# Kernel tuning notes

Hardware: AMD Instinct MI355X
Metric: run time of the kernel (lower is better)

The kernel has to match this reference:

```python
import jax, jax.numpy as jnp
import numpy as np

N, IN_F, OUT_F = 8192, 512, 128
NEG = -1e11
LRELU_SLOPE = 0.01  # torch nn.LeakyReLU default


def setup_inputs() -> dict:
    key = jax.random.key(0)
    k1, k2, k3, k4, k5 = jax.random.split(key, 5)
    h = jax.random.normal(k1, (N, IN_F), dtype=jnp.float32)
    adj = jax.random.randint(k2, (N, N), 0, 2, dtype=jnp.int32)
    # nn.Linear weights, [out, in] convention; kaiming-uniform-ish init
    w = jax.random.uniform(k3, (OUT_F, IN_F), dtype=jnp.float32,
                           minval=-1.0, maxval=1.0) / np.sqrt(IN_F)
    a1 = jax.random.uniform(k4, (1, OUT_F), dtype=jnp.float32,
                            minval=-1.0, maxval=1.0) / np.sqrt(OUT_F)
    a2 = jax.random.uniform(k5, (1, OUT_F), dtype=jnp.float32,
                            minval=-1.0, maxval=1.0) / np.sqrt(OUT_F)
    return {"h": h, "adj": adj, "w": w, "a1": a1, "a2": a2}


def reference(h, adj, w, a1, a2):
    wh = h @ w.T                                # [N, out]
    wh1 = wh @ a1.T                             # [N, 1]
    wh2 = wh @ a2.T                             # [N, 1]
    e = wh1 + wh2.T                             # [N, N] broadcast add
    e = jnp.where(e > 0, e, LRELU_SLOPE * e)    # leaky relu
    scores = jnp.where(adj > 0, e, jnp.float32(NEG))
    attention = jax.nn.softmax(scores, axis=-1)  # [N, N]
    h_new = attention @ wh                       # [N, out]
    return jax.nn.elu(h_new)
```

## Files before the change

kernel.cpp:

```cpp
#include <hip/hip_runtime.h>
#include <hip/hip_bf16.h>
#include <cstdint>
#include <cstddef>

#define NV    8192
#define KIN   512
#define MOUT  128
#define LOG2E 1.4426950408889634f

typedef __attribute__((ext_vector_type(4))) float f32x4;
typedef __attribute__((ext_vector_type(8))) short short8;

__device__ __forceinline__ float elu1(float x) { return x > 0.f ? x : expm1f(x); }

__device__ __forceinline__ unsigned int pkbf2(float a, float b) {
  union { __hip_bfloat162 h2; unsigned int u; } r;
  r.h2 = __float22bfloat162_rn(make_float2(a, b));
  return r.u;
}

__global__ __launch_bounds__(256) void k_wh(const float* __restrict__ h,
                                            const float* __restrict__ w,
                                            const float* __restrict__ a1,
                                            const float* __restrict__ a2,
                                            unsigned short* __restrict__ fragB,
                                            float* __restrict__ wh1,
                                            float* __restrict__ wh2) {
  __shared__ __align__(16) float hT[64][36];
  __shared__ __align__(16) float wT[64][128];
  const int t = threadIdx.x;
  const int row0 = blockIdx.x * 32;
  const int hr = t >> 3, hu = t & 7;
  const int wc = t >> 1, whalf = t & 1;
  const int cg = t & 31, rg = t >> 5;
  const int c0 = cg * 4, r0 = rg * 4;
  float acc[4][4] = {};

  for (int kt = 0; kt < 8; ++kt) {
    const int k0 = kt * 64;
    __syncthreads();
#pragma unroll
    for (int v = 0; v < 8; ++v)
      hT[hu + 8 * v][hr] = h[(size_t)(row0 + hr) * KIN + k0 + hu + 8 * v];
#pragma unroll
    for (int mv = 0; mv < 8; ++mv) {
      const float4 wv4 = *(const float4*)&w[(size_t)wc * KIN + k0 + whalf * 32 + mv * 4];
      wT[whalf * 32 + mv * 4 + 0][wc] = wv4.x;
      wT[whalf * 32 + mv * 4 + 1][wc] = wv4.y;
      wT[whalf * 32 + mv * 4 + 2][wc] = wv4.z;
      wT[whalf * 32 + mv * 4 + 3][wc] = wv4.w;
    }
    __syncthreads();
#pragma unroll 8
    for (int kk = 0; kk < 64; ++kk) {
      const float4 hv = *(const float4*)&hT[kk][r0];
      const float4 wv4 = *(const float4*)&wT[kk][c0];
      const float hvv[4] = {hv.x, hv.y, hv.z, hv.w};
      const float wvv[4] = {wv4.x, wv4.y, wv4.z, wv4.w};
#pragma unroll
      for (int i = 0; i < 4; ++i)
#pragma unroll
        for (int j = 0; j < 4; ++j)
          acc[i][j] = fmaf(hvv[i], wvv[j], acc[i][j]);
    }
  }

  {
    const size_t jt = (size_t)(row0 >> 6);
    const int ks = (row0 >> 5) & 1;
    const int lg = rg >> 1, ebase = (rg & 1) * 4;
    const int cgf = cg >> 2;
    const size_t fbase = (((jt * 8 + cgf) * 2 + ks) * 64 + lg * 16) * 8 + ebase;
#pragma unroll
    for (int j = 0; j < 4; ++j) {
      const int l15 = (cg & 3) * 4 + j;
      uint2 o;
      o.x = pkbf2(acc[0][j], acc[1][j]);
      o.y = pkbf2(acc[2][j], acc[3][j]);
      *(uint2*)&fragB[fbase + (size_t)l15 * 8] = o;
    }
  }

  const float4 a1v = *(const float4*)&a1[c0];
  const float4 a2v = *(const float4*)&a2[c0];
#pragma unroll
  for (int i = 0; i < 4; ++i) {
    float s1 = acc[i][0] * a1v.x + acc[i][1] * a1v.y + acc[i][2] * a1v.z + acc[i][3] * a1v.w;
    float s2 = acc[i][0] * a2v.x + acc[i][1] * a2v.y + acc[i][2] * a2v.z + acc[i][3] * a2v.w;
#pragma unroll
    for (int off = 16; off > 0; off >>= 1) {
      s1 += __shfl_down(s1, off, 32);
      s2 += __shfl_down(s2, off, 32);
    }
    if (cg == 0) {
      wh1[row0 + r0 + i] = s1 * LOG2E;
      wh2[row0 + r0 + i] = s2 * LOG2E;
    }
  }
}

__global__ __launch_bounds__(256) void k_attn_p(const unsigned short* __restrict__ fragB,
                                                const int* __restrict__ adj,
                                                const float* __restrict__ wh1l,
                                                const float* __restrict__ wh2l,
                                                float* __restrict__ out_p,
                                                float* __restrict__ psum_p,
                                                int ntiles) {
  __shared__ char smask[64 * 136];
  const int t = threadIdx.x;
  const int i0 = blockIdx.x * 64;
  const int jbase = blockIdx.y * ntiles * 64;
  const int lane = t & 63, wv = t >> 6;
  const int ih = wv & 1, ch = wv >> 1;
  const int l15 = lane & 15, lg = lane >> 4;
  const int mstride = ntiles * 8 + 8;

  const int* abase = adj + (size_t)i0 * NV + jbase;

  if (ntiles == 16) {
    for (int rr = 0; rr < 16; ++rr) {
      const int r = wv * 16 + rr;
      const int* rp = abase + (size_t)r * NV + lane * 16;
      unsigned int m = 0;
#pragma unroll
      for (int p = 0; p < 4; ++p) {
        const int4 v = *(const int4*)(rp + p * 4);
        m |= ((unsigned)(v.x & 1) << (4 * p))     | ((unsigned)(v.y & 1) << (4 * p + 1)) |
             ((unsigned)(v.z & 1) << (4 * p + 2)) | ((unsigned)(v.w & 1) << (4 * p + 3));
      }
      *(unsigned short*)&smask[r * 136 + (lane >> 2) * 8 + (lane & 3) * 2] = (unsigned short)m;
    }
  } else {
    for (int rr = 0; rr < 16; ++rr) {
      const int r = wv * 16 + rr;
      const int* rp = abase + (size_t)r * NV + lane * 8;
      unsigned int m = 0;
#pragma unroll
      for (int p = 0; p < 2; ++p) {
        const int4 v = *(const int4*)(rp + p * 4);
        m |= ((unsigned)(v.x & 1) << (4 * p))     | ((unsigned)(v.y & 1) << (4 * p + 1)) |
             ((unsigned)(v.z & 1) << (4 * p + 2)) | ((unsigned)(v.w & 1) << (4 * p + 3));
      }
      smask[r * 72 + lane] = (char)m;
    }
  }
  __syncthreads();

  const int rb = ih * 32;
  const float wh1a = wh1l[i0 + rb + l15];
  const float wh1b = wh1l[i0 + rb + 16 + l15];
  const char* mrowa = smask + (rb + l15) * mstride;
  const char* mrowb = smask + (rb + 16 + l15) * mstride;
  const unsigned short* bptr = fragB + (size_t)(jbase >> 6) * 8192 + ch * 4096 + lane * 8;
  const float* w2ptr = wh2l + jbase + lg * 8;

  f32x4 acc[2][4] = {};
  f32x4 accs[2] = {};
  short8 onesf;
#pragma unroll
  for (int e = 0; e < 8; ++e) onesf[e] = (short)0x3F80;

  uint2 m2a = *(const uint2*)&mrowa[0];
  uint2 m2b = *(const uint2*)&mrowb[0];
  short8 bf[8];
#pragma unroll
  for (int ks = 0; ks < 2; ++ks)
#pragma unroll
    for (int cgl = 0; cgl < 4; ++cgl)
      bf[ks * 4 + cgl] = *(const short8*)(bptr + cgl * 1024 + ks * 512);
  bptr += 8192;

  for (int it = 0; it < ntiles; ++it) {
    const unsigned int m16a = ((m2a.x >> (8 * lg)) & 0xFFu) |
                              (((m2a.y >> (8 * lg)) & 0xFFu) << 8);
    const unsigned int m16b = ((m2b.x >> (8 * lg)) & 0xFFu) |
                              (((m2b.y >> (8 * lg)) & 0xFFu) << 8);
    const float4 wq0 = *(const float4*)(w2ptr);
    const float4 wq1 = *(const float4*)(w2ptr + 4);
    const float4 wq2 = *(const float4*)(w2ptr + 32);
    const float4 wq3 = *(const float4*)(w2ptr + 36);
    w2ptr += 64;

    short8 afa[2], afb[2];
#pragma unroll
    for (int ks = 0; ks < 2; ++ks) {
      const float4 wa = ks ? wq2 : wq0;
      const float4 wb = ks ? wq3 : wq1;
      const float w2v[8] = {wa.x, wa.y, wa.z, wa.w, wb.x, wb.y, wb.z, wb.w};
      union { short8 s8; unsigned int u[4]; } pka, pkb;
#pragma unroll
      for (int e = 0; e < 4; ++e) {
        const float x0 = wh1a + w2v[2 * e];
        const float x1 = wh1a + w2v[2 * e + 1];
        const float y0 = wh1b + w2v[2 * e];
        const float y1 = wh1b + w2v[2 * e + 1];
        const float lx0 = fmaxf(x0, 0.01f * x0);
        const float lx1 = fmaxf(x1, 0.01f * x1);
        const float ly0 = fmaxf(y0, 0.01f * y0);
        const float ly1 = fmaxf(y1, 0.01f * y1);
        float px0 = __builtin_amdgcn_exp2f(lx0);
        float px1 = __builtin_amdgcn_exp2f(lx1);
        float py0 = __builtin_amdgcn_exp2f(ly0);
        float py1 = __builtin_amdgcn_exp2f(ly1);
        px0 = ((m16a >> (ks * 8 + 2 * e)) & 1u) ? px0 : 0.f;
        px1 = ((m16a >> (ks * 8 + 2 * e + 1)) & 1u) ? px1 : 0.f;
        py0 = ((m16b >> (ks * 8 + 2 * e)) & 1u) ? py0 : 0.f;
        py1 = ((m16b >> (ks * 8 + 2 * e + 1)) & 1u) ? py1 : 0.f;
        pka.u[e] = pkbf2(px0, px1);
        pkb.u[e] = pkbf2(py0, py1);
      }
      afa[ks] = pka.s8;
      afb[ks] = pkb.s8;
    }
    if (it + 1 < ntiles) {
      m2a = *(const uint2*)&mrowa[(it + 1) * 8];
      m2b = *(const uint2*)&mrowb[(it + 1) * 8];
    }
#pragma unroll
    for (int ks = 0; ks < 2; ++ks) {
      acc[0][0] = __builtin_amdgcn_mfma_f32_16x16x32_bf16(afa[ks], bf[ks * 4 + 0], acc[0][0], 0, 0, 0);
      acc[0][1] = __builtin_amdgcn_mfma_f32_16x16x32_bf16(afa[ks], bf[ks * 4 + 1], acc[0][1], 0, 0, 0);
      acc[0][2] = __builtin_amdgcn_mfma_f32_16x16x32_bf16(afa[ks], bf[ks * 4 + 2], acc[0][2], 0, 0, 0);
      acc[0][3] = __builtin_amdgcn_mfma_f32_16x16x32_bf16(afa[ks], bf[ks * 4 + 3], acc[0][3], 0, 0, 0);
      accs[0]   = __builtin_amdgcn_mfma_f32_16x16x32_bf16(afa[ks], onesf, accs[0], 0, 0, 0);
      acc[1][0] = __builtin_amdgcn_mfma_f32_16x16x32_bf16(afb[ks], bf[ks * 4 + 0], acc[1][0], 0, 0, 0);
      acc[1][1] = __builtin_amdgcn_mfma_f32_16x16x32_bf16(afb[ks], bf[ks * 4 + 1], acc[1][1], 0, 0, 0);
      acc[1][2] = __builtin_amdgcn_mfma_f32_16x16x32_bf16(afb[ks], bf[ks * 4 + 2], acc[1][2], 0, 0, 0);
      acc[1][3] = __builtin_amdgcn_mfma_f32_16x16x32_bf16(afb[ks], bf[ks * 4 + 3], acc[1][3], 0, 0, 0);
      accs[1]   = __builtin_amdgcn_mfma_f32_16x16x32_bf16(afb[ks], onesf, accs[1], 0, 0, 0);
    }
    if (it + 1 < ntiles) {
#pragma unroll
      for (int ks = 0; ks < 2; ++ks)
#pragma unroll
        for (int cgl = 0; cgl < 4; ++cgl)
          bf[ks * 4 + cgl] = *(const short8*)(bptr + cgl * 1024 + ks * 512);
      bptr += 8192;
    }
  }

  if (ch == 0 && l15 == 0) {
#pragma unroll
    for (int rg = 0; rg < 2; ++rg)
#pragma unroll
      for (int r = 0; r < 4; ++r)
        psum_p[(size_t)blockIdx.y * NV + i0 + rb + rg * 16 + lg * 4 + r] = accs[rg][r];
  }

#pragma unroll
  for (int rg = 0; rg < 2; ++rg) {
    const size_t ob = ((size_t)blockIdx.y * NV + i0 + rb + rg * 16) * MOUT + ch * 64;
#pragma unroll
    for (int cgl = 0; cgl < 4; ++cgl)
#pragma unroll
      for (int r = 0; r < 4; ++r)
        out_p[ob + (size_t)(lg * 4 + r) * MOUT + cgl * 16 + l15] = acc[rg][cgl][r];
  }
}

__global__ __launch_bounds__(256) void k_comb(const float* __restrict__ out_p,
                                              const float* __restrict__ psum_p,
                                              float* __restrict__ out, int S) {
  const int idx = (blockIdx.x * 256 + threadIdx.x) * 4;
  const int n = idx >> 7;
  float denom = 0.f;
  for (int s = 0; s < S; ++s) denom += psum_p[(size_t)s * NV + n];
  float4 acc = {0.f, 0.f, 0.f, 0.f};
  for (int s = 0; s < S; ++s) {
    const float4 v = *(const float4*)&out_p[(size_t)s * NV * MOUT + idx];
    acc.x += v.x; acc.y += v.y; acc.z += v.z; acc.w += v.w;
  }
  const float inv = 1.f / denom;
  float4 o;
  o.x = elu1(acc.x * inv);
  o.y = elu1(acc.y * inv);
  o.z = elu1(acc.z * inv);
  o.w = elu1(acc.w * inv);
  *(float4*)&out[idx] = o;
}

extern "C" void kernel_launch(void* const* d_in, const int* in_sizes, int n_in,
                              void* d_out, int out_size, void* d_ws, size_t ws_size,
                              hipStream_t stream) {
  const float* h  = (const float*)d_in[0];
  const int* adj  = (const int*)d_in[1];
  const float* w  = (const float*)d_in[2];
  const float* a1 = (const float*)d_in[3];
  const float* a2 = (const float*)d_in[4];
  float* out = (float*)d_out;

  char* ws = (char*)d_ws;
  unsigned short* fragB = (unsigned short*)ws;
  size_t off = (size_t)MOUT * NV * 2;
  float* wh1 = (float*)(ws + off); off += (size_t)NV * 4;
  float* wh2 = (float*)(ws + off); off += (size_t)NV * 4;
  float* psum_p = (float*)(ws + off); off += (size_t)16 * NV * 4;
  float* out_p = (float*)(ws + off);

  int S = 16;
  while (S > 8 && off + (size_t)S * NV * MOUT * 4 > ws_size) S >>= 1;
  const int ntiles = 128 / S;

  k_wh<<<NV / 32, 256, 0, stream>>>(h, w, a1, a2, fragB, wh1, wh2);
  k_attn_p<<<dim3(NV / 64, S), 256, 0, stream>>>(fragB, adj, wh1, wh2, out_p, psum_p, ntiles);
  k_comb<<<(NV * MOUT / 4) / 256, 256, 0, stream>>>(out_p, psum_p, out, S);
}
```

Measured before the change: 134.5 us.

## Fix split-K to 8 with 1D grid, batch adjacency loads, prefetch wh2

Hardcodes the j-dimension split at 8 partitions (16 tiles each) and remaps blocks onto a 1D grid so the splits of a row block are adjacent. This halves the partial output and denominator traffic written by the attention kernel and read by the combine kernel. The adjacency mask build now issues loads for two rows before packing them, which raises memory-level parallelism. The wh2 values are prefetched one tile ahead. Fewer blocks could reduce latency hiding.

Measured after the change: 139.1 us. 3.4% more time.

```diff
diff --git a/kernel.cpp b/kernel.cpp
--- a/kernel.cpp
+++ b/kernel.cpp
@@ -104,53 +104,47 @@
                                                 const float* __restrict__ wh1l,
                                                 const float* __restrict__ wh2l,
                                                 float* __restrict__ out_p,
-                                                float* __restrict__ psum_p,
-                                                int ntiles) {
+                                                float* __restrict__ psum_p) {
   __shared__ char smask[64 * 136];
   const int t = threadIdx.x;
-  const int i0 = blockIdx.x * 64;
-  const int jbase = blockIdx.y * ntiles * 64;
+  const int bid = blockIdx.x;
+  const int y = bid & 7;
+  const int i0 = (bid >> 3) * 64;
+  const int jbase = y * 1024;
   const int lane = t & 63, wv = t >> 6;
   const int ih = wv & 1, ch = wv >> 1;
   const int l15 = lane & 15, lg = lane >> 4;
-  const int mstride = ntiles * 8 + 8;
 
   const int* abase = adj + (size_t)i0 * NV + jbase;
 
-  if (ntiles == 16) {
-    for (int rr = 0; rr < 16; ++rr) {
-      const int r = wv * 16 + rr;
-      const int* rp = abase + (size_t)r * NV + lane * 16;
-      unsigned int m = 0;
-#pragma unroll
-      for (int p = 0; p < 4; ++p) {
-        const int4 v = *(const int4*)(rp + p * 4);
-        m |= ((unsigned)(v.x & 1) << (4 * p))     | ((unsigned)(v.y & 1) << (4 * p + 1)) |
-             ((unsigned)(v.z & 1) << (4 * p + 2)) | ((unsigned)(v.w & 1) << (4 * p + 3));
-      }
-      *(unsigned short*)&smask[r * 136 + (lane >> 2) * 8 + (lane & 3) * 2] = (unsigned short)m;
-    }
-  } else {
-    for (int rr = 0; rr < 16; ++rr) {
-      const int r = wv * 16 + rr;
-      const int* rp = abase + (size_t)r * NV + lane * 8;
-      unsigned int m = 0;
-#pragma unroll
-      for (int p = 0; p < 2; ++p) {
-        const int4 v = *(const int4*)(rp + p * 4);
-        m |= ((unsigned)(v.x & 1) << (4 * p))     | ((unsigned)(v.y & 1) << (4 * p + 1)) |
-             ((unsigned)(v.z & 1) << (4 * p + 2)) | ((unsigned)(v.w & 1) << (4 * p + 3));
-      }
-      smask[r * 72 + lane] = (char)m;
-    }
+  for (int rr = 0; rr < 16; rr += 2) {
+    const int r0w = wv * 16 + rr;
+    const int* rp0 = abase + (size_t)r0w * NV + lane * 16;
+    const int* rp1 = rp0 + NV;
+    int4 v0[4], v1[4];
+#pragma unroll
+    for (int p = 0; p < 4; ++p) v0[p] = *(const int4*)(rp0 + p * 4);
+#pragma unroll
+    for (int p = 0; p < 4; ++p) v1[p] = *(const int4*)(rp1 + p * 4);
+    unsigned int m0 = 0, m1 = 0;
+#pragma unroll
+    for (int p = 0; p < 4; ++p) {
+      m0 |= ((unsigned)(v0[p].x & 1) << (4 * p))     | ((unsigned)(v0[p].y & 1) << (4 * p + 1)) |
+            ((unsigned)(v0[p].z & 1) << (4 * p + 2)) | ((unsigned)(v0[p].w & 1) << (4 * p + 3));
+      m1 |= ((unsigned)(v1[p].x & 1) << (4 * p))     | ((unsigned)(v1[p].y & 1) << (4 * p + 1)) |
+            ((unsigned)(v1[p].z & 1) << (4 * p + 2)) | ((unsigned)(v1[p].w & 1) << (4 * p + 3));
+    }
+    const int off = (lane >> 2) * 8 + (lane & 3) * 2;
+    *(unsigned short*)&smask[(r0w) * 136 + off] = (unsigned short)m0;
+    *(unsigned short*)&smask[(r0w + 1) * 136 + off] = (unsigned short)m1;
   }
   __syncthreads();
 
   const int rb = ih * 32;
   const float wh1a = wh1l[i0 + rb + l15];
   const float wh1b = wh1l[i0 + rb + 16 + l15];
-  const char* mrowa = smask + (rb + l15) * mstride;
-  const char* mrowb = smask + (rb + 16 + l15) * mstride;
+  const char* mrowa = smask + (rb + l15) * 136;
+  const char* mrowb = smask + (rb + 16 + l15) * 136;
   const unsigned short* bptr = fragB + (size_t)(jbase >> 6) * 8192 + ch * 4096 + lane * 8;
   const float* w2ptr = wh2l + jbase + lg * 8;
 
@@ -162,6 +156,11 @@
 
   uint2 m2a = *(const uint2*)&mrowa[0];
   uint2 m2b = *(const uint2*)&mrowb[0];
+  float4 wq0 = *(const float4*)(w2ptr);
+  float4 wq1 = *(const float4*)(w2ptr + 4);
+  float4 wq2 = *(const float4*)(w2ptr + 32);
+  float4 wq3 = *(const float4*)(w2ptr + 36);
+  w2ptr += 64;
   short8 bf[8];
 #pragma unroll
   for (int ks = 0; ks < 2; ++ks)
@@ -170,17 +169,11 @@
       bf[ks * 4 + cgl] = *(const short8*)(bptr + cgl * 1024 + ks * 512);
   bptr += 8192;
 
-  for (int it = 0; it < ntiles; ++it) {
+  for (int it = 0; it < 16; ++it) {
     const unsigned int m16a = ((m2a.x >> (8 * lg)) & 0xFFu) |
                               (((m2a.y >> (8 * lg)) & 0xFFu) << 8);
     const unsigned int m16b = ((m2b.x >> (8 * lg)) & 0xFFu) |
                               (((m2b.y >> (8 * lg)) & 0xFFu) << 8);
-    const float4 wq0 = *(const float4*)(w2ptr);
-    const float4 wq1 = *(const float4*)(w2ptr + 4);
-    const float4 wq2 = *(const float4*)(w2ptr + 32);
-    const float4 wq3 = *(const float4*)(w2ptr + 36);
-    w2ptr += 64;
-
     short8 afa[2], afb[2];
 #pragma unroll
     for (int ks = 0; ks < 2; ++ks) {
@@ -212,9 +205,14 @@
       afa[ks] = pka.s8;
       afb[ks] = pkb.s8;
     }
-    if (it + 1 < ntiles) {
+    if (it + 1 < 16) {
       m2a = *(const uint2*)&mrowa[(it + 1) * 8];
       m2b = *(const uint2*)&mrowb[(it + 1) * 8];
+      wq0 = *(const float4*)(w2ptr);
+      wq1 = *(const float4*)(w2ptr + 4);
+      wq2 = *(const float4*)(w2ptr + 32);
+      wq3 = *(const float4*)(w2ptr + 36);
+      w2ptr += 64;
     }
 #pragma unroll
     for (int ks = 0; ks < 2; ++ks) {
@@ -229,7 +227,7 @@
       acc[1][3] = __builtin_amdgcn_mfma_f32_16x16x32_bf16(afb[ks], bf[ks * 4 + 3], acc[1][3], 0, 0, 0);
       accs[1]   = __builtin_amdgcn_mfma_f32_16x16x32_bf16(afb[ks], onesf, accs[1], 0, 0, 0);
     }
-    if (it + 1 < ntiles) {
+    if (it + 1 < 16) {
 #pragma unroll
       for (int ks = 0; ks < 2; ++ks)
 #pragma unroll
@@ -244,12 +242,12 @@
     for (int rg = 0; rg < 2; ++rg)
 #pragma unroll
       for (int r = 0; r < 4; ++r)
-        psum_p[(size_t)blockIdx.y * NV + i0 + rb + rg * 16 + lg * 4 + r] = accs[rg][r];
+        psum_p[(size_t)y * NV + i0 + rb + rg * 16 + lg * 4 + r] = accs[rg][r];
   }
 
 #pragma unroll
   for (int rg = 0; rg < 2; ++rg) {
-    const size_t ob = ((size_t)blockIdx.y * NV + i0 + rb + rg * 16) * MOUT + ch * 64;
+    const size_t ob = ((size_t)y * NV + i0 + rb + rg * 16) * MOUT + ch * 64;
 #pragma unroll
     for (int cgl = 0; cgl < 4; ++cgl)
 #pragma unroll
@@ -294,14 +292,10 @@
   size_t off = (size_t)MOUT * NV * 2;
   float* wh1 = (float*)(ws + off); off += (size_t)NV * 4;
   float* wh2 = (float*)(ws + off); off += (size_t)NV * 4;
-  float* psum_p = (float*)(ws + off); off += (size_t)16 * NV * 4;
+  float* psum_p = (float*)(ws + off); off += (size_t)8 * NV * 4;
   float* out_p = (float*)(ws + off);
 
-  int S = 16;
-  while (S > 8 && off + (size_t)S * NV * MOUT * 4 > ws_size) S >>= 1;
-  const int ntiles = 128 / S;
-
   k_wh<<<NV / 32, 256, 0, stream>>>(h, w, a1, a2, fragB, wh1, wh2);
-  k_attn_p<<<dim3(NV / 64, S), 256, 0, stream>>>(fragB, adj, wh1, wh2, out_p, psum_p, ntiles);
-  k_comb<<<(NV * MOUT / 4) / 256, 256, 0, stream>>>(out_p, psum_p, out, S);
-}
+  k_attn_p<<<1024, 256, 0, stream>>>(fragB, adj, wh1, wh2, out_p, psum_p);
+  k_comb<<<(NV * MOUT / 4) / 256, 256, 0, stream>>>(out_p, psum_p, out, 8);
+}
```

## Fuse split-K combine into attention kernel via last-block atomic counter

Applied to the files above, without the earlier changes.

Removes the separate combine kernel: each attention block increments a per-row-tile atomic counter, and the last of the 8 column splits sums the partial outputs and denominators, then applies ELU. The split count is fixed at 8 with 16 tiles per block, which drops the workspace-dependent path. The projection kernel is halved to 16 rows per block for more blocks and uses vectorized h loads. This saves a launch and lets the reduction overlap other blocks' work, at the cost of threadfence and atomic overhead and serialized tail work in the last blocks.

After: 172.6 us. +28.3%, slower.

```diff
diff --git a/kernel.cpp b/kernel.cpp
--- a/kernel.cpp
+++ b/kernel.cpp
@@ -25,23 +25,30 @@
                                             const float* __restrict__ a2,
                                             unsigned short* __restrict__ fragB,
                                             float* __restrict__ wh1,
-                                            float* __restrict__ wh2) {
-  __shared__ __align__(16) float hT[64][36];
+                                            float* __restrict__ wh2,
+                                            int* __restrict__ cnt) {
+  __shared__ __align__(16) float hT[64][18];
   __shared__ __align__(16) float wT[64][128];
   const int t = threadIdx.x;
-  const int row0 = blockIdx.x * 32;
-  const int hr = t >> 3, hu = t & 7;
+  const int row0 = blockIdx.x * 16;
+  const int hrow = t & 15, hkq = t >> 4;
   const int wc = t >> 1, whalf = t & 1;
   const int cg = t & 31, rg = t >> 5;
-  const int c0 = cg * 4, r0 = rg * 4;
-  float acc[4][4] = {};
+  const int c0 = cg * 4, r0 = rg * 2;
+  float acc[2][4] = {};
+
+  if (blockIdx.x == 0 && t < 128) cnt[t] = 0;
 
   for (int kt = 0; kt < 8; ++kt) {
     const int k0 = kt * 64;
     __syncthreads();
-#pragma unroll
-    for (int v = 0; v < 8; ++v)
-      hT[hu + 8 * v][hr] = h[(size_t)(row0 + hr) * KIN + k0 + hu + 8 * v];
+    {
+      const float4 hv = *(const float4*)&h[(size_t)(row0 + hrow) * KIN + k0 + hkq * 4];
+      hT[hkq * 4 + 0][hrow] = hv.x;
+      hT[hkq * 4 + 1][hrow] = hv.y;
+      hT[hkq * 4 + 2][hrow] = hv.z;
+      hT[hkq * 4 + 3][hrow] = hv.w;
+    }
 #pragma unroll
     for (int mv = 0; mv < 8; ++mv) {
       const float4 wv4 = *(const float4*)&w[(size_t)wc * KIN + k0 + whalf * 32 + mv * 4];
@@ -53,12 +60,12 @@
     __syncthreads();
 #pragma unroll 8
     for (int kk = 0; kk < 64; ++kk) {
-      const float4 hv = *(const float4*)&hT[kk][r0];
+      const float2 hv = *(const float2*)&hT[kk][r0];
       const float4 wv4 = *(const float4*)&wT[kk][c0];
-      const float hvv[4] = {hv.x, hv.y, hv.z, hv.w};
+      const float hvv[2] = {hv.x, hv.y};
       const float wvv[4] = {wv4.x, wv4.y, wv4.z, wv4.w};
 #pragma unroll
-      for (int i = 0; i < 4; ++i)
+      for (int i = 0; i < 2; ++i)
 #pragma unroll
         for (int j = 0; j < 4; ++j)
           acc[i][j] = fmaf(hvv[i], wvv[j], acc[i][j]);
@@ -68,23 +75,21 @@
   {
     const size_t jt = (size_t)(row0 >> 6);
     const int ks = (row0 >> 5) & 1;
-    const int lg = rg >> 1, ebase = (rg & 1) * 4;
+    const int lg = (((row0 & 31) + rg * 2) >> 3);
     const int cgf = cg >> 2;
-    const size_t fbase = (((jt * 8 + cgf) * 2 + ks) * 64 + lg * 16) * 8 + ebase;
+    unsigned int* fB32 = (unsigned int*)fragB;
+    const size_t ubase = (((jt * 8 + cgf) * 2 + ks) * 64 + lg * 16) * 4 + (rg & 3);
 #pragma unroll
     for (int j = 0; j < 4; ++j) {
       const int l15 = (cg & 3) * 4 + j;
-      uint2 o;
-      o.x = pkbf2(acc[0][j], acc[1][j]);
-      o.y = pkbf2(acc[2][j], acc[3][j]);
-      *(uint2*)&fragB[fbase + (size_t)l15 * 8] = o;
+      fB32[ubase + (size_t)l15 * 4] = pkbf2(acc[0][j], acc[1][j]);
     }
   }
 
   const float4 a1v = *(const float4*)&a1[c0];
   const float4 a2v = *(const float4*)&a2[c0];
 #pragma unroll
-  for (int i = 0; i < 4; ++i) {
+  for (int i = 0; i < 2; ++i) {
     float s1 = acc[i][0] * a1v.x + acc[i][1] * a1v.y + acc[i][2] * a1v.z + acc[i][3] * a1v.w;
     float s2 = acc[i][0] * a2v.x + acc[i][1] * a2v.y + acc[i][2] * a2v.z + acc[i][3] * a2v.w;
 #pragma unroll
@@ -105,52 +110,40 @@
                                                 const float* __restrict__ wh2l,
                                                 float* __restrict__ out_p,
                                                 float* __restrict__ psum_p,
-                                                int ntiles) {
+                                                float* __restrict__ out,
+                                                int* __restrict__ cnt) {
   __shared__ char smask[64 * 136];
+  __shared__ float invden[64];
+  __shared__ int lastf;
   const int t = threadIdx.x;
-  const int i0 = blockIdx.x * 64;
-  const int jbase = blockIdx.y * ntiles * 64;
+  const int x = blockIdx.x;
+  const int i0 = x * 64;
+  const int jbase = blockIdx.y * 1024;
   const int lane = t & 63, wv = t >> 6;
   const int ih = wv & 1, ch = wv >> 1;
   const int l15 = lane & 15, lg = lane >> 4;
-  const int mstride = ntiles * 8 + 8;
 
   const int* abase = adj + (size_t)i0 * NV + jbase;
 
-  if (ntiles == 16) {
-    for (int rr = 0; rr < 16; ++rr) {
-      const int r = wv * 16 + rr;
-      const int* rp = abase + (size_t)r * NV + lane * 16;
-      unsigned int m = 0;
-#pragma unroll
-      for (int p = 0; p < 4; ++p) {
-        const int4 v = *(const int4*)(rp + p * 4);
-        m |= ((unsigned)(v.x & 1) << (4 * p))     | ((unsigned)(v.y & 1) << (4 * p + 1)) |
-             ((unsigned)(v.z & 1) << (4 * p + 2)) | ((unsigned)(v.w & 1) << (4 * p + 3));
-      }
-      *(unsigned short*)&smask[r * 136 + (lane >> 2) * 8 + (lane & 3) * 2] = (unsigned short)m;
-    }
-  } else {
-    for (int rr = 0; rr < 16; ++rr) {
-      const int r = wv * 16 + rr;
-      const int* rp = abase + (size_t)r * NV + lane * 8;
-      unsigned int m = 0;
-#pragma unroll
-      for (int p = 0; p < 2; ++p) {
-        const int4 v = *(const int4*)(rp + p * 4);
-        m |= ((unsigned)(v.x & 1) << (4 * p))     | ((unsigned)(v.y & 1) << (4 * p + 1)) |
-             ((unsigned)(v.z & 1) << (4 * p + 2)) | ((unsigned)(v.w & 1) << (4 * p + 3));
-      }
-      smask[r * 72 + lane] = (char)m;
-    }
+  for (int rr = 0; rr < 16; ++rr) {
+    const int r = wv * 16 + rr;
+    const int* rp = abase + (size_t)r * NV + lane * 16;
+    unsigned int m = 0;
+#pragma unroll
+    for (int p = 0; p < 4; ++p) {
+      const int4 v = *(const int4*)(rp + p * 4);
+      m |= ((unsigned)(v.x & 1) << (4 * p))     | ((unsigned)(v.y & 1) << (4 * p + 1)) |
+           ((unsigned)(v.z & 1) << (4 * p + 2)) | ((unsigned)(v.w & 1) << (4 * p + 3));
+    }
+    *(unsigned short*)&smask[r * 136 + (lane >> 2) * 8 + (lane & 3) * 2] = (unsigned short)m;
   }
   __syncthreads();
 
   const int rb = ih * 32;
   const float wh1a = wh1l[i0 + rb + l15];
   const float wh1b = wh1l[i0 + rb + 16 + l15];
-  const char* mrowa = smask + (rb + l15) * mstride;
-  const char* mrowb = smask + (rb + 16 + l15) * mstride;
+  const char* mrowa = smask + (rb + l15) * 136;
+  const char* mrowb = smask + (rb + 16 + l15) * 136;
   const unsigned short* bptr = fragB + (size_t)(jbase >> 6) * 8192 + ch * 4096 + lane * 8;
   const float* w2ptr = wh2l + jbase + lg * 8;
 
@@ -170,7 +163,7 @@
       bf[ks * 4 + cgl] = *(const short8*)(bptr + cgl * 1024 + ks * 512);
   bptr += 8192;
 
-  for (int it = 0; it < ntiles; ++it) {
+  for (int it = 0; it < 16; ++it) {
     const unsigned int m16a = ((m2a.x >> (8 * lg)) & 0xFFu) |
                               (((m2a.y >> (8 * lg)) & 0xFFu) << 8);
     const unsigned int m16b = ((m2b.x >> (8 * lg)) & 0xFFu) |
@@ -212,7 +205,7 @@
       afa[ks] = pka.s8;
       afb[ks] = pkb.s8;
     }
-    if (it + 1 < ntiles) {
+    if (it + 1 < 16) {
       m2a = *(const uint2*)&mrowa[(it + 1) * 8];
       m2b = *(const uint2*)&mrowb[(it + 1) * 8];
     }
@@ -229,7 +222,7 @@
       acc[1][3] = __builtin_amdgcn_mfma_f32_16x16x32_bf16(afb[ks], bf[ks * 4 + 3], acc[1][3], 0, 0, 0);
       accs[1]   = __builtin_amdgcn_mfma_f32_16x16x32_bf16(afb[ks], onesf, accs[1], 0, 0, 0);
     }
-    if (it + 1 < ntiles) {
+    if (it + 1 < 16) {
 #pragma unroll
       for (int ks = 0; ks < 2; ++ks)
 #pragma unroll
@@ -246,7 +239,6 @@
       for (int r = 0; r < 4; ++r)
         psum_p[(size_t)blockIdx.y * NV + i0 + rb + rg * 16 + lg * 4 + r] = accs[rg][r];
   }
-
 #pragma unroll
   for (int rg = 0; rg < 2; ++rg) {
     const size_t ob = ((size_t)blockIdx.y * NV + i0 + rb + rg * 16) * MOUT + ch * 64;
@@ -256,27 +248,39 @@
       for (int r = 0; r < 4; ++r)
         out_p[ob + (size_t)(lg * 4 + r) * MOUT + cgl * 16 + l15] = acc[rg][cgl][r];
   }
-}
-
-__global__ __launch_bounds__(256) void k_comb(const float* __restrict__ out_p,
-                                              const float* __restrict__ psum_p,
-                                              float* __restrict__ out, int S) {
-  const int idx = (blockIdx.x * 256 + threadIdx.x) * 4;
-  const int n = idx >> 7;
-  float denom = 0.f;
-  for (int s = 0; s < S; ++s) denom += psum_p[(size_t)s * NV + n];
-  float4 acc = {0.f, 0.f, 0.f, 0.f};
-  for (int s = 0; s < S; ++s) {
-    const float4 v = *(const float4*)&out_p[(size_t)s * NV * MOUT + idx];
-    acc.x += v.x; acc.y += v.y; acc.z += v.z; acc.w += v.w;
-  }
-  const float inv = 1.f / denom;
-  float4 o;
-  o.x = elu1(acc.x * inv);
-  o.y = elu1(acc.y * inv);
-  o.z = elu1(acc.z * inv);
-  o.w = elu1(acc.w * inv);
-  *(float4*)&out[idx] = o;
+
+  __syncthreads();
+  if (t == 0) {
+    __threadfence();
+    lastf = (atomicAdd(&cnt[x], 1) == 7);
+  }
+  __syncthreads();
+  if (!lastf) return;
+  __threadfence();
+
+  if (t < 64) {
+    float d = 0.f;
+    for (int s = 0; s < 8; ++s) d += psum_p[(size_t)s * NV + i0 + t];
+    invden[t] = 1.f / d;
+  }
+  __syncthreads();
+#pragma unroll
+  for (int k = 0; k < 8; ++k) {
+    const int idx4 = k * 256 + t;
+    const int row = idx4 >> 5, c4 = (idx4 & 31) * 4;
+    float4 a = {0.f, 0.f, 0.f, 0.f};
+    for (int s = 0; s < 8; ++s) {
+      const float4 v = *(const float4*)&out_p[((size_t)s * NV + i0 + row) * MOUT + c4];
+      a.x += v.x; a.y += v.y; a.z += v.z; a.w += v.w;
+    }
+    const float inv = invden[row];
+    float4 o;
+    o.x = elu1(a.x * inv);
+    o.y = elu1(a.y * inv);
+    o.z = elu1(a.z * inv);
+    o.w = elu1(a.w * inv);
+    *(float4*)&out[(size_t)(i0 + row) * MOUT + c4] = o;
+  }
 }
 
 extern "C" void kernel_launch(void* const* d_in, const int* in_sizes, int n_in,
@@ -294,14 +298,10 @@
   size_t off = (size_t)MOUT * NV * 2;
   float* wh1 = (float*)(ws + off); off += (size_t)NV * 4;
   float* wh2 = (float*)(ws + off); off += (size_t)NV * 4;
-  float* psum_p = (float*)(ws + off); off += (size_t)16 * NV * 4;
+  float* psum_p = (float*)(ws + off); off += (size_t)8 * NV * 4;
+  int* cnt = (int*)(ws + off); off += 1024;
   float* out_p = (float*)(ws + off);
 
-  int S = 16;
-  while (S > 8 && off + (size_t)S * NV * MOUT * 4 > ws_size) S >>= 1;
-  const int ntiles = 128 / S;
-
-  k_wh<<<NV / 32, 256, 0, stream>>>(h, w, a1, a2, fragB, wh1, wh2);
-  k_attn_p<<<dim3(NV / 64, S), 256, 0, stream>>>(fragB, adj, wh1, wh2, out_p, psum_p, ntiles);
-  k_comb<<<(NV * MOUT / 4) / 256, 256, 0, stream>>>(out_p, psum_p, out, S);
+  k_wh<<<NV / 16, 256, 0, stream>>>(h, w, a1, a2, fragB, wh1, wh2, cnt);
+  k_attn_p<<<dim3(NV / 64, 8), 256, 0, stream>>>(fragB, adj, wh1, wh2, out_p, psum_p, out, cnt);
 }
```
